# Kernel optimization log

Hardware: AMD Instinct MI355X
Metric: run time of the kernel (lower is better)

The kernel has to match this reference:

```python
import jax, jax.numpy as jnp
import numpy as np


def setup_inputs() -> dict:
    key = jax.random.key(0)
    k1, k2, k3, k4 = jax.random.split(key, 4)
    B, C, H, W = 8, 64, 64, 64
    Cr = C // 8
    x = jax.random.normal(k1, (B, C, H, W), dtype=jnp.float32)
    Wf = jax.random.normal(k2, (Cr, C), dtype=jnp.float32) * (1.0 / np.sqrt(C))
    Wg = jax.random.normal(k3, (Cr, C), dtype=jnp.float32) * (1.0 / np.sqrt(C))
    Wh = jax.random.normal(k4, (C, C), dtype=jnp.float32) * (1.0 / np.sqrt(C))
    gamma = jnp.zeros((1,), dtype=jnp.float32)
    return {"x": x, "Wf": Wf, "Wg": Wg, "Wh": Wh, "gamma": gamma}


def reference(x, Wf, Wg, Wh, gamma):
    B, C, H, W = x.shape
    N = H * W
    xf = x.reshape(B, C, N)                      # [B, C, N]
    fx = jnp.einsum("oc,bcn->bno", Wf, xf)       # queries [B, N, C/8]
    gx = jnp.einsum("oc,bcn->bon", Wg, xf)       # keys    [B, C/8, N]
    hx = jnp.einsum("oc,bcn->bon", Wh, xf)       # values  [B, C,   N]
    beta = jnp.einsum("bnd,bdm->bnm", fx, gx)    # [B, N, N], no 1/sqrt(d) scale (SAGAN)
    beta = jax.nn.softmax(beta, axis=-1)
    # o = bmm(hx, beta^T): o[b,c,i] = sum_j hx[b,c,j] * beta[b,i,j]
    o = jnp.einsum("bcj,bij->bci", hx, beta)     # [B, C, N]
    o = o.reshape(B, C, H, W)
    return gamma * o + x
```

## Files before the change

### kernel.cpp

```cpp
#include <hip/hip_runtime.h>
#include <hip/hip_bf16.h>


#define N_ 4096
#define LOG2E 1.4426950408889634f

typedef __attribute__((ext_vector_type(8)))  __bf16 bf16x8;
typedef __attribute__((ext_vector_type(4)))  float  f32x4;
typedef __attribute__((ext_vector_type(16))) float  f32x16;

union U16B { uint4 u; bf16x8 b; };

static __device__ inline uint pack_bf2(float a, float b) {
  __hip_bfloat162 h = __float22bfloat162_rn(make_float2(a, b));
  uint r; __builtin_memcpy(&r, &h, 4); return r;
}
static __device__ inline ushort f2bf(float a) {
  __hip_bfloat16 h = __float2bfloat16(a);
  ushort r; __builtin_memcpy(&r, &h, 2); return r;
}

__global__ __launch_bounds__(256) void transpose_kernel(
    const float* __restrict__ x, ushort* __restrict__ xT, uint* __restrict__ zb)
{
  __shared__ float T[64 * 65];
  const int b = blockIdx.y, n0 = blockIdx.x * 64, tid = threadIdx.x;
  if (blockIdx.x == 0 && blockIdx.y == 0 && tid < 16) zb[tid] = 0u;
  const int nl = tid & 63, cw = tid >> 6;
#pragma unroll
  for (int i = 0; i < 16; ++i) {
    const int c = i * 4 + cw;
    T[c * 65 + nl] = x[((size_t)(b * 64 + c)) * N_ + n0 + nl];
  }
  __syncthreads();
  const int n = tid >> 2, cq = (tid & 3) * 16;
  uint o[8];
#pragma unroll
  for (int j = 0; j < 8; ++j)
    o[j] = pack_bf2(T[(cq + 2 * j) * 65 + n], T[(cq + 2 * j + 1) * 65 + n]);
  ushort* dst = xT + ((size_t)(b * N_ + n0 + n)) * 64 + cq;
  *(uint4*)dst       = make_uint4(o[0], o[1], o[2], o[3]);
  *(uint4*)(dst + 8) = make_uint4(o[4], o[5], o[6], o[7]);
}

__global__ __launch_bounds__(256) void proj_kernel(
    const ushort* __restrict__ xT, const float* __restrict__ Wf,
    const float* __restrict__ Wg,  const float* __restrict__ Wh,
    ushort* __restrict__ Qp, ushort* __restrict__ Kp, ushort* __restrict__ VT)
{
  __shared__ __align__(16) ushort Wb[80 * 72];
  const int b = blockIdx.y, nb = blockIdx.x * 64, tid = threadIdx.x;
#pragma unroll
  for (int i = 0; i < 20; ++i) {
    const int e = i * 256 + tid;
    const int row = e >> 6, col = e & 63;
    float v;
    if (row < 8)       v = Wf[row * 64 + col] * LOG2E;
    else if (row < 16) v = Wg[(row - 8) * 64 + col];
    else               v = Wh[(row - 16) * 64 + col];
    Wb[row * 72 + col] = f2bf(v);
  }
  __syncthreads();
  const int l = tid & 63, w = tid >> 6;
  const int l15 = l & 15, lq = l >> 4;
  const int n = nb + w * 16 + l15;
  const ushort* xb = xT + ((size_t)(b * N_ + n)) * 64 + lq * 8;
  U16B bf0, bf1;
  bf0.u = *(const uint4*)xb;
  bf1.u = *(const uint4*)(xb + 32);
  f32x4 acc[5];
#pragma unroll
  for (int mt = 0; mt < 5; ++mt) {
    U16B a0, a1;
    a0.u = *(const uint4*)(Wb + (mt * 16 + l15) * 72 + lq * 8);
    a1.u = *(const uint4*)(Wb + (mt * 16 + l15) * 72 + 32 + lq * 8);
    f32x4 c0 = __builtin_amdgcn_mfma_f32_16x16x32_bf16(a0.b, bf0.b, (f32x4){0.f,0.f,0.f,0.f}, 0, 0, 0);
    acc[mt]  = __builtin_amdgcn_mfma_f32_16x16x32_bf16(a1.b, bf1.b, c0, 0, 0, 0);
  }
  {
    uint lo = pack_bf2(acc[0][0], acc[0][1]);
    uint hi = pack_bf2(acc[0][2], acc[0][3]);
    ushort* dst = (lq < 2 ? Qp : Kp) + ((size_t)(b * N_ + n)) * 8 + (lq & 1) * 4;
    *(uint2*)dst = make_uint2(lo, hi);
  }
#pragma unroll
  for (int mt = 1; mt < 5; ++mt)
#pragma unroll
    for (int r = 0; r < 4; ++r) {
      const int c = (mt - 1) * 16 + lq * 4 + r;
      VT[((size_t)(b * 64 + c)) * N_ + n] = f2bf(acc[mt][r]);
    }
}

__global__ __launch_bounds__(256) void attn_kernel(
    const ushort* __restrict__ Qp, const ushort* __restrict__ Kp,
    const ushort* __restrict__ VT, const uint* __restrict__ zb,
    float* __restrict__ Opart, float* __restrict__ Lpart)
{
  __shared__ __align__(16) char smem[46080];
  const int b = blockIdx.z, jh = blockIdx.y;
  const int q0 = blockIdx.x * 128;
  const int tid = threadIdx.x, w = tid >> 6, l = tid & 63;
  const int l15 = l & 15, lq = l >> 4, l31 = l & 31, lq1 = l >> 5;
  const int qw = q0 + w * 32;
  char* Pw = smem + 27648 + w * 4608;
  const uint4* zb16 = (const uint4*)zb;

  U16B qf0, qf1;
  qf0.u = *(const uint4*)(Qp + ((size_t)(b * N_ + qw + l15)) * 8);
  qf1.u = *(const uint4*)(Qp + ((size_t)(b * N_ + qw + 16 + l15)) * 8);

  const int jbase = jh * 2048;
  const int sc = tid >> 2, sj = (tid & 3) * 2;
  const ushort* Vsrc = VT + ((size_t)(b * 64 + sc)) * N_ + jbase + sj * 8;
  const int ws0 = sc * 144 + (((sj)     ^ (sc >> 3)) & 7) * 16;
  const int ws1 = sc * 144 + (((sj + 1) ^ (sc >> 3)) & 7) * 16;

  U16B kf[4], kfn[4];
#pragma unroll
  for (int t = 0; t < 4; ++t) {
    const uint4* ka = (l < 16)
        ? (const uint4*)(Kp + ((size_t)(b * N_ + jbase + t * 16 + l15)) * 8) : zb16;
    kf[t].u = *ka;
  }
  uint4 v0 = *(const uint4*)Vsrc;
  uint4 v1 = *(const uint4*)(Vsrc + 8);
  *(uint4*)(smem + ws0) = v0;
  *(uint4*)(smem + ws1) = v1;
  __syncthreads();

  f32x16 O0 = {0,0,0,0,0,0,0,0,0,0,0,0,0,0,0,0};
  f32x16 O1 = {0,0,0,0,0,0,0,0,0,0,0,0,0,0,0,0};
  float L0 = 0.f, L1 = 0.f;

  int cur = 0;
  for (int jt = 0; jt < 32; ++jt) {
    const int nxt = (cur == 2) ? 0 : cur + 1;
    if (jt < 31) {
      const int jn = jbase + (jt + 1) * 64;
#pragma unroll
      for (int t = 0; t < 4; ++t) {
        const uint4* ka = (l < 16)
            ? (const uint4*)(Kp + ((size_t)(b * N_ + jn + t * 16 + l15)) * 8) : zb16;
        kfn[t].u = *ka;
      }
      v0 = *(const uint4*)(Vsrc + (jt + 1) * 64);
      v1 = *(const uint4*)(Vsrc + (jt + 1) * 64 + 8);
    }
    f32x4 St0[4], St1[4];
#pragma unroll
    for (int t = 0; t < 4; ++t) {
      St0[t] = __builtin_amdgcn_mfma_f32_16x16x32_bf16(kf[t].b, qf0.b, (f32x4){0.f,0.f,0.f,0.f}, 0, 0, 0);
      St1[t] = __builtin_amdgcn_mfma_f32_16x16x32_bf16(kf[t].b, qf1.b, (f32x4){0.f,0.f,0.f,0.f}, 0, 0, 0);
    }
#pragma unroll
    for (int u = 0; u < 2; ++u) {
      const int prow = u * 16 + l15;
      const int rot = prow >> 3;
      char* base = Pw + prow * 144 + (lq & 1) * 8;
#pragma unroll
      for (int t = 0; t < 4; ++t) {
        const f32x4 s = u ? St1[t] : St0[t];
        const float p0 = __builtin_amdgcn_exp2f(s[0]);
        const float p1 = __builtin_amdgcn_exp2f(s[1]);
        const float p2 = __builtin_amdgcn_exp2f(s[2]);
        const float p3 = __builtin_amdgcn_exp2f(s[3]);
        const float ps = (p0 + p1) + (p2 + p3);
        if (u) L1 += ps; else L0 += ps;
        const int slot = ((t * 2 + (lq >> 1)) ^ rot) & 7;
        *(uint2*)(base + slot * 16) = make_uint2(pack_bf2(p0, p1), pack_bf2(p2, p3));
      }
    }
    const char* Vb = smem + cur * 9216;
#pragma unroll
    for (int ks = 0; ks < 4; ++ks) {
      U16B pa;
      pa.u = *(const uint4*)(Pw + l31 * 144 + (((ks * 2 + lq1) ^ (l31 >> 3)) & 7) * 16);
      {
        const int c = l31;
        U16B vb; vb.u = *(const uint4*)(Vb + c * 144 + (((ks * 2 + lq1) ^ (c >> 3)) & 7) * 16);
        O0 = __builtin_amdgcn_mfma_f32_32x32x16_bf16(pa.b, vb.b, O0, 0, 0, 0);
      }
      {
        const int c = 32 + l31;
        U16B vb; vb.u = *(const uint4*)(Vb + c * 144 + (((ks * 2 + lq1) ^ (c >> 3)) & 7) * 16);
        O1 = __builtin_amdgcn_mfma_f32_32x32x16_bf16(pa.b, vb.b, O1, 0, 0, 0);
      }
    }
    if (jt < 31) {
      char* Vn = smem + nxt * 9216;
      *(uint4*)(Vn + ws0) = v0;
      *(uint4*)(Vn + ws1) = v1;
#pragma unroll
      for (int t = 0; t < 4; ++t) kf[t] = kfn[t];
    }
    __syncthreads();
    cur = nxt;
  }

  L0 += __shfl_xor(L0, 16); L0 += __shfl_xor(L0, 32);
  L1 += __shfl_xor(L1, 16); L1 += __shfl_xor(L1, 32);
  float* Lp = Lpart + ((size_t)(jh * 8 + b)) * N_;
  if (lq == 0) Lp[qw + l15] = L0;
  if (lq == 1) Lp[qw + 16 + l15] = L1;

  float* Ob = Opart + (((size_t)(jh * 8 + b)) * N_ + qw) * 64;
#pragma unroll
  for (int g = 0; g < 4; ++g)
#pragma unroll
    for (int rr = 0; rr < 4; ++rr) {
      const int qp = rr + 8 * g + 4 * lq1;
      Ob[qp * 64 + l31]      = O0[g * 4 + rr];
      Ob[qp * 64 + 32 + l31] = O1[g * 4 + rr];
    }
}

__global__ __launch_bounds__(256) void combine_kernel(
    const float* __restrict__ Opart, const float* __restrict__ Lpart,
    const float* __restrict__ x, const float* __restrict__ gamma,
    float* __restrict__ out)
{
  __shared__ float T[64 * 65];
  const int b = blockIdx.y, n0 = blockIdx.x * 64, tid = threadIdx.x;
  const float g = gamma[0];
  const float* O0 = Opart + ((size_t)(b) * N_ + n0) * 64;
  const float* O1 = Opart + ((size_t)(8 + b) * N_ + n0) * 64;
#pragma unroll
  for (int i = 0; i < 16; ++i) {
    const int idx = i * 256 + tid;
    const int n = idx >> 6, c = idx & 63;
    T[n * 65 + c] = O0[idx] + O1[idx];
  }
  __syncthreads();
  const int n = tid & 63, cq = (tid >> 6) * 16;
  const float l0 = Lpart[(size_t)(b) * N_ + n0 + n];
  const float l1 = Lpart[(size_t)(8 + b) * N_ + n0 + n];
  const float gr = g / (l0 + l1);
#pragma unroll
  for (int i = 0; i < 16; ++i) {
    const int c = cq + i;
    const size_t oi = ((size_t)(b * 64 + c)) * N_ + n0 + n;
    out[oi] = gr * T[n * 65 + c] + x[oi];
  }
}

extern "C" void kernel_launch(void* const* d_in, const int* in_sizes, int n_in,
                              void* d_out, int out_size, void* d_ws, size_t ws_size,
                              hipStream_t stream) {
  const float* x     = (const float*)d_in[0];
  const float* Wf    = (const float*)d_in[1];
  const float* Wg    = (const float*)d_in[2];
  const float* Wh    = (const float*)d_in[3];
  const float* gamma = (const float*)d_in[4];
  float* out = (float*)d_out;
  char* ws = (char*)d_ws;

  ushort* Qp    = (ushort*)(ws);
  ushort* Kp    = (ushort*)(ws + 512 * 1024);
  ushort* VT    = (ushort*)(ws + 1024 * 1024);
  uint*   zb    = (uint*)  (ws + 5 * 1024 * 1024);
  float*  Opart = (float*) (ws + 6 * 1024 * 1024);
  float*  Lpart = (float*) (ws + 22 * 1024 * 1024);
  ushort* xT    = (ushort*)(ws + 6 * 1024 * 1024);

  transpose_kernel<<<dim3(64, 8), 256, 0, stream>>>(x, xT, zb);
  proj_kernel     <<<dim3(64, 8), 256, 0, stream>>>(xT, Wf, Wg, Wh, Qp, Kp, VT);
  attn_kernel     <<<dim3(32, 2, 8), 256, 0, stream>>>(Qp, Kp, VT, zb, Opart, Lpart);
  combine_kernel  <<<dim3(64, 8), 256, 0, stream>>>(Opart, Lpart, x, gamma, out);
}
```

Measured before the change: 128.3 us.

## Fuse transpose into projection, pre-swizzle V fragments, split keys four ways

Merges the transpose and projection kernels so the bf16 transposed x stays in LDS instead of going through global memory. Projection now writes V in a fragment-ready tiled layout, so the attention kernel reads V operands straight from global/L2 with no LDS staging or block barriers. The key range is split into four chunks instead of two for more blocks, and the partial outputs are stored as bf16 to halve combine traffic. This gives up LDS reuse of V across waves and adds bf16 rounding of the partial sums.

```diff
diff --git a/kernel.cpp b/kernel.cpp
--- a/kernel.cpp
+++ b/kernel.cpp
@@ -19,55 +19,63 @@
   __hip_bfloat16 h = __float2bfloat16(a);
   ushort r; __builtin_memcpy(&r, &h, 2); return r;
 }
-
-__global__ __launch_bounds__(256) void transpose_kernel(
-    const float* __restrict__ x, ushort* __restrict__ xT, uint* __restrict__ zb)
+static __device__ inline float bflo(uint u) {
+  uint v = u << 16; float f; __builtin_memcpy(&f, &v, 4); return f;
+}
+static __device__ inline float bfhi(uint u) {
+  uint v = u & 0xffff0000u; float f; __builtin_memcpy(&f, &v, 4); return f;
+}
+
+__global__ __launch_bounds__(256) void prep_kernel(
+    const float* __restrict__ x,  const float* __restrict__ Wf,
+    const float* __restrict__ Wg, const float* __restrict__ Wh,
+    ushort* __restrict__ Qp, ushort* __restrict__ Kp,
+    ushort* __restrict__ Vf, uint* __restrict__ zb)
 {
-  __shared__ float T[64 * 65];
+  __shared__ __align__(16) char smem[37376];
+  float*  T   = (float*)smem;
+  ushort* xTl = (ushort*)(smem + 16640);
+  ushort* Wb  = (ushort*)(smem + 25856);
   const int b = blockIdx.y, n0 = blockIdx.x * 64, tid = threadIdx.x;
-  if (blockIdx.x == 0 && blockIdx.y == 0 && tid < 16) zb[tid] = 0u;
-  const int nl = tid & 63, cw = tid >> 6;
-#pragma unroll
-  for (int i = 0; i < 16; ++i) {
-    const int c = i * 4 + cw;
-    T[c * 65 + nl] = x[((size_t)(b * 64 + c)) * N_ + n0 + nl];
-  }
-  __syncthreads();
-  const int n = tid >> 2, cq = (tid & 3) * 16;
-  uint o[8];
-#pragma unroll
-  for (int j = 0; j < 8; ++j)
-    o[j] = pack_bf2(T[(cq + 2 * j) * 65 + n], T[(cq + 2 * j + 1) * 65 + n]);
-  ushort* dst = xT + ((size_t)(b * N_ + n0 + n)) * 64 + cq;
-  *(uint4*)dst       = make_uint4(o[0], o[1], o[2], o[3]);
-  *(uint4*)(dst + 8) = make_uint4(o[4], o[5], o[6], o[7]);
-}
-
-__global__ __launch_bounds__(256) void proj_kernel(
-    const ushort* __restrict__ xT, const float* __restrict__ Wf,
-    const float* __restrict__ Wg,  const float* __restrict__ Wh,
-    ushort* __restrict__ Qp, ushort* __restrict__ Kp, ushort* __restrict__ VT)
-{
-  __shared__ __align__(16) ushort Wb[80 * 72];
-  const int b = blockIdx.y, nb = blockIdx.x * 64, tid = threadIdx.x;
-#pragma unroll
-  for (int i = 0; i < 20; ++i) {
-    const int e = i * 256 + tid;
-    const int row = e >> 6, col = e & 63;
-    float v;
-    if (row < 8)       v = Wf[row * 64 + col] * LOG2E;
-    else if (row < 16) v = Wg[(row - 8) * 64 + col];
-    else               v = Wh[(row - 16) * 64 + col];
-    Wb[row * 72 + col] = f2bf(v);
-  }
-  __syncthreads();
-  const int l = tid & 63, w = tid >> 6;
-  const int l15 = l & 15, lq = l >> 4;
-  const int n = nb + w * 16 + l15;
-  const ushort* xb = xT + ((size_t)(b * N_ + n)) * 64 + lq * 8;
+  if (blockIdx.x == 0 && b == 0 && tid < 16) zb[tid] = 0u;
+
+  {
+    const int nl = tid & 63, cw = tid >> 6;
+#pragma unroll
+    for (int i = 0; i < 16; ++i) {
+      const int c = i * 4 + cw;
+      T[c * 65 + nl] = x[((size_t)(b * 64 + c)) * N_ + n0 + nl];
+    }
+  }
+  {
+#pragma unroll
+    for (int i = 0; i < 20; ++i) {
+      const int e = i * 256 + tid;
+      const int row = e >> 6, col = e & 63;
+      float v;
+      if (row < 8)       v = Wf[row * 64 + col] * LOG2E;
+      else if (row < 16) v = Wg[(row - 8) * 64 + col];
+      else               v = Wh[(row - 16) * 64 + col];
+      Wb[row * 72 + col] = f2bf(v);
+    }
+  }
+  __syncthreads();
+  {
+    const int n = tid >> 2, cq = (tid & 3) * 16;
+    uint o[8];
+#pragma unroll
+    for (int j = 0; j < 8; ++j)
+      o[j] = pack_bf2(T[(cq + 2 * j) * 65 + n], T[(cq + 2 * j + 1) * 65 + n]);
+    *(uint4*)(xTl + n * 72 + cq)     = make_uint4(o[0], o[1], o[2], o[3]);
+    *(uint4*)(xTl + n * 72 + cq + 8) = make_uint4(o[4], o[5], o[6], o[7]);
+  }
+  __syncthreads();
+
+  const int l = tid & 63, w = tid >> 6, l15 = l & 15, lq = l >> 4;
+  const int nn = w * 16 + l15;
   U16B bf0, bf1;
-  bf0.u = *(const uint4*)xb;
-  bf1.u = *(const uint4*)(xb + 32);
+  bf0.u = *(const uint4*)(xTl + nn * 72 + lq * 8);
+  bf1.u = *(const uint4*)(xTl + nn * 72 + 32 + lq * 8);
   f32x4 acc[5];
 #pragma unroll
   for (int mt = 0; mt < 5; ++mt) {
@@ -77,75 +85,65 @@
     f32x4 c0 = __builtin_amdgcn_mfma_f32_16x16x32_bf16(a0.b, bf0.b, (f32x4){0.f,0.f,0.f,0.f}, 0, 0, 0);
     acc[mt]  = __builtin_amdgcn_mfma_f32_16x16x32_bf16(a1.b, bf1.b, c0, 0, 0, 0);
   }
+  const int n = n0 + nn;
   {
     uint lo = pack_bf2(acc[0][0], acc[0][1]);
     uint hi = pack_bf2(acc[0][2], acc[0][3]);
     ushort* dst = (lq < 2 ? Qp : Kp) + ((size_t)(b * N_ + n)) * 8 + (lq & 1) * 4;
     *(uint2*)dst = make_uint2(lo, hi);
   }
+  ushort* Vt = (ushort*)smem;
 #pragma unroll
   for (int mt = 1; mt < 5; ++mt)
 #pragma unroll
     for (int r = 0; r < 4; ++r) {
       const int c = (mt - 1) * 16 + lq * 4 + r;
-      VT[((size_t)(b * 64 + c)) * N_ + n] = f2bf(acc[mt][r]);
-    }
+      Vt[(c >> 5) * 2048 + w * 512 + ((l15 >> 3) * 32 + (c & 31)) * 8 + (l15 & 7)]
+          = f2bf(acc[mt][r]);
+    }
+  __syncthreads();
+  const uint4* src = (const uint4*)Vt;
+  uint4* dst = (uint4*)(Vf + ((size_t)(b * 64 + blockIdx.x)) * 4096);
+  dst[tid]       = src[tid];
+  dst[256 + tid] = src[256 + tid];
 }
 
 __global__ __launch_bounds__(256) void attn_kernel(
     const ushort* __restrict__ Qp, const ushort* __restrict__ Kp,
-    const ushort* __restrict__ VT, const uint* __restrict__ zb,
-    float* __restrict__ Opart, float* __restrict__ Lpart)
+    const ushort* __restrict__ Vf, const uint* __restrict__ zb,
+    ushort* __restrict__ Opart, float* __restrict__ Lpart)
 {
-  __shared__ __align__(16) char smem[46080];
-  const int b = blockIdx.z, jh = blockIdx.y;
-  const int q0 = blockIdx.x * 128;
+  __shared__ __align__(16) char smem[32768];
+  const int b = blockIdx.z, js = blockIdx.y, q0 = blockIdx.x * 128;
   const int tid = threadIdx.x, w = tid >> 6, l = tid & 63;
   const int l15 = l & 15, lq = l >> 4, l31 = l & 31, lq1 = l >> 5;
   const int qw = q0 + w * 32;
-  char* Pw = smem + 27648 + w * 4608;
   const uint4* zb16 = (const uint4*)zb;
 
   U16B qf0, qf1;
   qf0.u = *(const uint4*)(Qp + ((size_t)(b * N_ + qw + l15)) * 8);
   qf1.u = *(const uint4*)(Qp + ((size_t)(b * N_ + qw + 16 + l15)) * 8);
 
-  const int jbase = jh * 2048;
-  const int sc = tid >> 2, sj = (tid & 3) * 2;
-  const ushort* Vsrc = VT + ((size_t)(b * 64 + sc)) * N_ + jbase + sj * 8;
-  const int ws0 = sc * 144 + (((sj)     ^ (sc >> 3)) & 7) * 16;
-  const int ws1 = sc * 144 + (((sj + 1) ^ (sc >> 3)) & 7) * 16;
+  const int pconst = (lq >> 1) * 512 + l15 * 16 + (lq & 1) * 8;
+  const int jt0 = js * 16;
 
   U16B kf[4], kfn[4];
 #pragma unroll
-  for (int t = 0; t < 4; ++t) {
-    const uint4* ka = (l < 16)
-        ? (const uint4*)(Kp + ((size_t)(b * N_ + jbase + t * 16 + l15)) * 8) : zb16;
-    kf[t].u = *ka;
-  }
-  uint4 v0 = *(const uint4*)Vsrc;
-  uint4 v1 = *(const uint4*)(Vsrc + 8);
-  *(uint4*)(smem + ws0) = v0;
-  *(uint4*)(smem + ws1) = v1;
-  __syncthreads();
+  for (int t = 0; t < 4; ++t)
+    kf[t].u = (l < 16)
+        ? *(const uint4*)(Kp + ((size_t)(b * N_ + jt0 * 64 + t * 16 + l15)) * 8)
+        : *zb16;
 
   f32x16 O0 = {0,0,0,0,0,0,0,0,0,0,0,0,0,0,0,0};
   f32x16 O1 = {0,0,0,0,0,0,0,0,0,0,0,0,0,0,0,0};
   float L0 = 0.f, L1 = 0.f;
 
-  int cur = 0;
-  for (int jt = 0; jt < 32; ++jt) {
-    const int nxt = (cur == 2) ? 0 : cur + 1;
-    if (jt < 31) {
-      const int jn = jbase + (jt + 1) * 64;
-#pragma unroll
-      for (int t = 0; t < 4; ++t) {
-        const uint4* ka = (l < 16)
-            ? (const uint4*)(Kp + ((size_t)(b * N_ + jn + t * 16 + l15)) * 8) : zb16;
-        kfn[t].u = *ka;
-      }
-      v0 = *(const uint4*)(Vsrc + (jt + 1) * 64);
-      v1 = *(const uint4*)(Vsrc + (jt + 1) * 64 + 8);
+  for (int jt = 0; jt < 16; ++jt) {
+    if (jt < 15) {
+      const size_t kr = (size_t)(b * N_ + (jt0 + jt + 1) * 64);
+#pragma unroll
+      for (int t = 0; t < 4; ++t)
+        kfn[t].u = (l < 16) ? *(const uint4*)(Kp + (kr + t * 16 + l15) * 8) : *zb16;
     }
     f32x4 St0[4], St1[4];
 #pragma unroll
@@ -153,11 +151,9 @@
       St0[t] = __builtin_amdgcn_mfma_f32_16x16x32_bf16(kf[t].b, qf0.b, (f32x4){0.f,0.f,0.f,0.f}, 0, 0, 0);
       St1[t] = __builtin_amdgcn_mfma_f32_16x16x32_bf16(kf[t].b, qf1.b, (f32x4){0.f,0.f,0.f,0.f}, 0, 0, 0);
     }
-#pragma unroll
-    for (int u = 0; u < 2; ++u) {
-      const int prow = u * 16 + l15;
-      const int rot = prow >> 3;
-      char* base = Pw + prow * 144 + (lq & 1) * 8;
+    char* Pp = smem + (((w << 1) | (jt & 1)) << 12);
+#pragma unroll
+    for (int u = 0; u < 2; ++u)
 #pragma unroll
       for (int t = 0; t < 4; ++t) {
         const f32x4 s = u ? St1[t] : St0[t];
@@ -167,75 +163,71 @@
         const float p3 = __builtin_amdgcn_exp2f(s[3]);
         const float ps = (p0 + p1) + (p2 + p3);
         if (u) L1 += ps; else L0 += ps;
-        const int slot = ((t * 2 + (lq >> 1)) ^ rot) & 7;
-        *(uint2*)(base + slot * 16) = make_uint2(pack_bf2(p0, p1), pack_bf2(p2, p3));
+        *(uint2*)(Pp + t * 1024 + u * 256 + pconst)
+            = make_uint2(pack_bf2(p0, p1), pack_bf2(p2, p3));
       }
-    }
-    const char* Vb = smem + cur * 9216;
+    const ushort* Vb = Vf + ((size_t)(b * 64 + jt0 + jt)) * 4096;
 #pragma unroll
     for (int ks = 0; ks < 4; ++ks) {
-      U16B pa;
-      pa.u = *(const uint4*)(Pw + l31 * 144 + (((ks * 2 + lq1) ^ (l31 >> 3)) & 7) * 16);
-      {
-        const int c = l31;
-        U16B vb; vb.u = *(const uint4*)(Vb + c * 144 + (((ks * 2 + lq1) ^ (c >> 3)) & 7) * 16);
-        O0 = __builtin_amdgcn_mfma_f32_32x32x16_bf16(pa.b, vb.b, O0, 0, 0, 0);
-      }
-      {
-        const int c = 32 + l31;
-        U16B vb; vb.u = *(const uint4*)(Vb + c * 144 + (((ks * 2 + lq1) ^ (c >> 3)) & 7) * 16);
-        O1 = __builtin_amdgcn_mfma_f32_32x32x16_bf16(pa.b, vb.b, O1, 0, 0, 0);
-      }
-    }
-    if (jt < 31) {
-      char* Vn = smem + nxt * 9216;
-      *(uint4*)(Vn + ws0) = v0;
-      *(uint4*)(Vn + ws1) = v1;
+      U16B pa; pa.u = *(const uint4*)(Pp + ks * 1024 + l * 16);
+      U16B v0; v0.u = *(const uint4*)(Vb + ks * 512 + l * 8);
+      O0 = __builtin_amdgcn_mfma_f32_32x32x16_bf16(pa.b, v0.b, O0, 0, 0, 0);
+      U16B v1; v1.u = *(const uint4*)(Vb + 2048 + ks * 512 + l * 8);
+      O1 = __builtin_amdgcn_mfma_f32_32x32x16_bf16(pa.b, v1.b, O1, 0, 0, 0);
+    }
+    if (jt < 15) {
 #pragma unroll
       for (int t = 0; t < 4; ++t) kf[t] = kfn[t];
     }
-    __syncthreads();
-    cur = nxt;
   }
 
   L0 += __shfl_xor(L0, 16); L0 += __shfl_xor(L0, 32);
   L1 += __shfl_xor(L1, 16); L1 += __shfl_xor(L1, 32);
-  float* Lp = Lpart + ((size_t)(jh * 8 + b)) * N_;
+  float* Lp = Lpart + ((size_t)(js * 8 + b)) * N_;
   if (lq == 0) Lp[qw + l15] = L0;
   if (lq == 1) Lp[qw + 16 + l15] = L1;
 
-  float* Ob = Opart + (((size_t)(jh * 8 + b)) * N_ + qw) * 64;
+  ushort* Op = Opart + (((size_t)(js * 8 + b)) * N_ + qw) * 64;
 #pragma unroll
   for (int g = 0; g < 4; ++g)
 #pragma unroll
     for (int rr = 0; rr < 4; ++rr) {
       const int qp = rr + 8 * g + 4 * lq1;
-      Ob[qp * 64 + l31]      = O0[g * 4 + rr];
-      Ob[qp * 64 + 32 + l31] = O1[g * 4 + rr];
+      Op[qp * 64 + l31]      = f2bf(O0[g * 4 + rr]);
+      Op[qp * 64 + 32 + l31] = f2bf(O1[g * 4 + rr]);
     }
 }
 
 __global__ __launch_bounds__(256) void combine_kernel(
-    const float* __restrict__ Opart, const float* __restrict__ Lpart,
+    const ushort* __restrict__ Opart, const float* __restrict__ Lpart,
     const float* __restrict__ x, const float* __restrict__ gamma,
     float* __restrict__ out)
 {
   __shared__ float T[64 * 65];
   const int b = blockIdx.y, n0 = blockIdx.x * 64, tid = threadIdx.x;
+  float acc[16];
+#pragma unroll
+  for (int e = 0; e < 16; ++e) acc[e] = 0.f;
+#pragma unroll
+  for (int js = 0; js < 4; ++js) {
+    const ushort* Op = Opart + (((size_t)(js * 8 + b)) * N_ + n0) * 64 + tid * 16;
+    uint4 a = *(const uint4*)Op;
+    uint4 c2 = *(const uint4*)(Op + 8);
+    acc[0] += bflo(a.x);  acc[1] += bfhi(a.x);  acc[2] += bflo(a.y);  acc[3] += bfhi(a.y);
+    acc[4] += bflo(a.z);  acc[5] += bfhi(a.z);  acc[6] += bflo(a.w);  acc[7] += bfhi(a.w);
+    acc[8] += bflo(c2.x); acc[9] += bfhi(c2.x); acc[10]+= bflo(c2.y); acc[11]+= bfhi(c2.y);
+    acc[12]+= bflo(c2.z); acc[13]+= bfhi(c2.z); acc[14]+= bflo(c2.w); acc[15]+= bfhi(c2.w);
+  }
+  const int nr = tid >> 2, c0 = (tid & 3) * 16;
+#pragma unroll
+  for (int e = 0; e < 16; ++e) T[nr * 65 + c0 + e] = acc[e];
+  __syncthreads();
   const float g = gamma[0];
-  const float* O0 = Opart + ((size_t)(b) * N_ + n0) * 64;
-  const float* O1 = Opart + ((size_t)(8 + b) * N_ + n0) * 64;
-#pragma unroll
-  for (int i = 0; i < 16; ++i) {
-    const int idx = i * 256 + tid;
-    const int n = idx >> 6, c = idx & 63;
-    T[n * 65 + c] = O0[idx] + O1[idx];
-  }
-  __syncthreads();
   const int n = tid & 63, cq = (tid >> 6) * 16;
-  const float l0 = Lpart[(size_t)(b) * N_ + n0 + n];
-  const float l1 = Lpart[(size_t)(8 + b) * N_ + n0 + n];
-  const float gr = g / (l0 + l1);
+  float Ls = 0.f;
+#pragma unroll
+  for (int js = 0; js < 4; ++js) Ls += Lpart[((size_t)(js * 8 + b)) * N_ + n0 + n];
+  const float gr = g / Ls;
 #pragma unroll
   for (int i = 0; i < 16; ++i) {
     const int c = cq + i;
@@ -257,14 +249,12 @@
 
   ushort* Qp    = (ushort*)(ws);
   ushort* Kp    = (ushort*)(ws + 512 * 1024);
-  ushort* VT    = (ushort*)(ws + 1024 * 1024);
+  ushort* Vf    = (ushort*)(ws + 1024 * 1024);
   uint*   zb    = (uint*)  (ws + 5 * 1024 * 1024);
-  float*  Opart = (float*) (ws + 6 * 1024 * 1024);
-  float*  Lpart = (float*) (ws + 22 * 1024 * 1024);
-  ushort* xT    = (ushort*)(ws + 6 * 1024 * 1024);
-
-  transpose_kernel<<<dim3(64, 8), 256, 0, stream>>>(x, xT, zb);
-  proj_kernel     <<<dim3(64, 8), 256, 0, stream>>>(xT, Wf, Wg, Wh, Qp, Kp, VT);
-  attn_kernel     <<<dim3(32, 2, 8), 256, 0, stream>>>(Qp, Kp, VT, zb, Opart, Lpart);
-  combine_kernel  <<<dim3(64, 8), 256, 0, stream>>>(Opart, Lpart, x, gamma, out);
-}
+  float*  Lpart = (float*) (ws + 5 * 1024 * 1024 + 1024);
+  ushort* Opart = (ushort*)(ws + 6 * 1024 * 1024);
+
+  prep_kernel   <<<dim3(64, 8),    256, 0, stream>>>(x, Wf, Wg, Wh, Qp, Kp, Vf, zb);
+  attn_kernel   <<<dim3(32, 4, 8), 256, 0, stream>>>(Qp, Kp, Vf, zb, Opart, Lpart);
+  combine_kernel<<<dim3(64, 8),    256, 0, stream>>>(Opart, Lpart, x, gamma, out);
+}
```

Measured after the change: 155.6 us. 21.2% more time.
